# Kernel tuning notes

Hardware: AMD Instinct MI355X
Metric: run time of the kernel (lower is better)

## Reference

```python
import jax, jax.numpy as jnp
import numpy as np

N_NODES = 50000
N_EDGES = 800000
N_GRAPHS = 256
IN_DIM, HIDDEN_DIM, EMBED_DIM = 128, 64, 128


def setup_inputs() -> dict:
    key = jax.random.key(0)
    ks = jax.random.split(key, 8)
    x = jax.random.normal(ks[0], (N_NODES, IN_DIM), dtype=jnp.float32)
    edge_index = jax.random.randint(ks[1], (2, N_EDGES), 0, N_NODES, dtype=jnp.int64)
    edge_weight = jax.random.uniform(ks[2], (N_EDGES,), dtype=jnp.float32)
    batch_vec = jnp.sort(jax.random.randint(ks[3], (N_NODES,), 0, N_GRAPHS, dtype=jnp.int64))
    # Glorot-ish params for the two GCNConv layers
    W1 = jax.random.normal(ks[4], (IN_DIM, HIDDEN_DIM), dtype=jnp.float32) / np.sqrt(IN_DIM)
    b1 = jnp.zeros((HIDDEN_DIM,), dtype=jnp.float32)
    W2 = jax.random.normal(ks[5], (HIDDEN_DIM, EMBED_DIM), dtype=jnp.float32) / np.sqrt(HIDDEN_DIM)
    b2 = jnp.zeros((EMBED_DIM,), dtype=jnp.float32)
    return {"x": x, "edge_index": edge_index, "edge_weight": edge_weight,
            "batch_vec": batch_vec, "W1": W1, "b1": b1, "W2": W2, "b2": b2}


def _gcn_conv(x, src, dst, ew, W, b, num_nodes):
    # PyG GCNConv: linear transform, add self-loops (weight 1), sym-normalize, aggregate at dst.
    h = x @ W  # [N, out]
    loops = jnp.arange(num_nodes, dtype=src.dtype)
    row = jnp.concatenate([src, loops])
    col = jnp.concatenate([dst, loops])
    w = jnp.concatenate([ew, jnp.ones((num_nodes,), x.dtype)])
    deg = jax.ops.segment_sum(w, col, num_segments=num_nodes)
    dis = jnp.where(deg > 0, jax.lax.rsqrt(deg), 0.0)  # deg^{-1/2}, inf -> 0
    norm = dis[row] * w * dis[col]  # [E+N]
    msg = h[row] * norm[:, None]  # gather + scale
    out = jax.ops.segment_sum(msg, col, num_segments=num_nodes)  # scatter-add
    return out + b


def reference(x, edge_index, edge_weight, batch_vec, W1, b1, W2, b2):
    src, dst = edge_index[0], edge_index[1]
    h = jax.nn.relu(_gcn_conv(x, src, dst, edge_weight, W1, b1, N_NODES))
    # dropout is identity at inference
    h = jax.nn.relu(_gcn_conv(h, src, dst, edge_weight, W2, b2, N_NODES))
    # global_mean_pool over graphs
    s = jax.ops.segment_sum(h, batch_vec, num_segments=N_GRAPHS)
    cnt = jax.ops.segment_sum(jnp.ones((N_NODES,), h.dtype), batch_vec, num_segments=N_GRAPHS)
    return s / jnp.maximum(cnt, 1.0)[:, None]
```

## Files before the change

kernel.cpp:

```cpp
#include <hip/hip_runtime.h>

constexpr int N_NODES  = 50000;
constexpr int N_EDGES  = 800000;
constexpr int N_GRAPHS = 256;
constexpr int IN_DIM   = 128;
constexpr int HID      = 64;
constexpr int EMB      = 128;
constexpr int NBKT     = 196;
constexpr int EB       = (N_EDGES + 1023) / 1024;
constexpr int GB       = (N_NODES + 31) / 32;
constexpr int GSB      = (N_NODES + 255) / 256;
constexpr int NB2      = 64;

constexpr size_t OFF_POOL  = 0;
constexpr size_t OFF_GST   = 32768;
constexpr size_t OFF_BBASE = 33026;
constexpr size_t OFF_DIS   = 33224;
constexpr size_t OFF_RS    = 83224;
constexpr size_t OFF_HCNT  = 133224;
constexpr size_t OFF_REC   = 286496;
constexpr size_t OFF_PART  = OFF_REC + 2 * (size_t)N_EDGES;
constexpr size_t OFF_H1    = OFF_PART;
constexpr size_t OFF_H1P   = OFF_PART + 4 * (size_t)N_EDGES;
constexpr size_t OFF_AGG2  = OFF_H1P;

__device__ inline unsigned bf16r(float f) {
    unsigned u = __float_as_uint(f);
    return (u + 0x7fffu + ((u >> 16) & 1u)) >> 16;
}
__device__ inline unsigned bf16pack2(float lo, float hi) {
    return bf16r(lo) | (bf16r(hi) << 16);
}
__device__ inline float bflo(unsigned v) { return __uint_as_float(v << 16); }
__device__ inline float bfhi(unsigned v) { return __uint_as_float(v & 0xffff0000u); }

__device__ inline void fma4(float4& acc, float s, const float4& v) {
    acc.x += s * v.x; acc.y += s * v.y; acc.z += s * v.z; acc.w += s * v.w;
}

__global__ __launch_bounds__(256) void k_p1(const int* __restrict__ dst,
                                            int* __restrict__ hcnt) {
    __shared__ int lh[NBKT];
    int tid = threadIdx.x;
    for (int i = tid; i < NBKT; i += 256) lh[i] = 0;
    __syncthreads();
    int base = blockIdx.x * 1024;
    #pragma unroll
    for (int j = 0; j < 4; ++j) {
        int e = base + j * 256 + tid;
        if (e < N_EDGES) atomicAdd(&lh[dst[e] >> 8], 1);
    }
    __syncthreads();
    for (int i = tid; i < NBKT; i += 256) hcnt[blockIdx.x * NBKT + i] = lh[i];
}

__global__ __launch_bounds__(256) void k_kab(const int* __restrict__ hcnt,
                                             int* __restrict__ bbase) {
    __shared__ int tile[256];
    int t = threadIdx.x;
    int v = 0;
    if (t < NBKT) {
        for (int i = 0; i < EB; ++i) v += hcnt[i * NBKT + t];
    }
    tile[t] = v;
    __syncthreads();
    for (int off = 1; off < 256; off <<= 1) {
        int a = (t >= off) ? tile[t - off] : 0;
        __syncthreads();
        tile[t] += a;
        __syncthreads();
    }
    if (t < NBKT) bbase[t] = tile[t] - v;
    if (t == NBKT - 1) bbase[NBKT] = tile[t];
}

__global__ __launch_bounds__(256) void k_kc(int* __restrict__ hcnt,
                                            const int* __restrict__ bbase,
                                            const int* __restrict__ batch,
                                            int* __restrict__ gstart) {
    __shared__ int tile[256];
    __shared__ int carry;
    int t = threadIdx.x;
    if (blockIdx.x < NBKT) {
        int b = blockIdx.x;
        if (t == 0) carry = bbase[b];
        __syncthreads();
        for (int i0 = 0; i0 < EB; i0 += 256) {
            int i = i0 + t;
            int v = (i < EB) ? hcnt[i * NBKT + b] : 0;
            tile[t] = v;
            __syncthreads();
            for (int off = 1; off < 256; off <<= 1) {
                int a = (t >= off) ? tile[t - off] : 0;
                __syncthreads();
                tile[t] += a;
                __syncthreads();
            }
            int incl = tile[t];
            if (i < EB) hcnt[i * NBKT + b] = carry + incl - v;
            __syncthreads();
            if (t == 255) carry += incl;
            __syncthreads();
        }
        return;
    }
    int i = (blockIdx.x - NBKT) * 256 + t;
    if (i >= N_NODES) return;
    int g = batch[i];
    if (i == 0) {
        for (int gg = 0; gg <= g; ++gg) gstart[gg] = 0;
    } else {
        int gp = batch[i - 1];
        for (int gg = gp + 1; gg <= g; ++gg) gstart[gg] = i;
    }
    if (i == N_NODES - 1) {
        for (int gg = g + 1; gg <= N_GRAPHS; ++gg) gstart[gg] = N_NODES;
    }
}

__global__ __launch_bounds__(256) void k_p2(const int* __restrict__ src,
                                            const int* __restrict__ dst,
                                            const float* __restrict__ ew,
                                            const int* __restrict__ hcnt,
                                            uint4* __restrict__ part) {
    __shared__ int lb[NBKT];
    __shared__ int lc[NBKT];
    int tid = threadIdx.x;
    for (int i = tid; i < NBKT; i += 256) {
        lb[i] = hcnt[blockIdx.x * NBKT + i];
        lc[i] = 0;
    }
    __syncthreads();
    int base = blockIdx.x * 1024;
    #pragma unroll
    for (int j = 0; j < 4; ++j) {
        int e = base + j * 256 + tid;
        if (e < N_EDGES) {
            int d = dst[e];
            int b = d >> 8;
            int r = atomicAdd(&lc[b], 1);
            part[lb[b] + r] = make_uint4((unsigned)src[e], (unsigned)d,
                                         __float_as_uint(ew[e]), 0u);
        }
    }
}

__global__ __launch_bounds__(256) void k_p3_gemm1(const uint4* __restrict__ part,
                                                  const int* __restrict__ bbase,
                                                  int* __restrict__ rs,
                                                  float* __restrict__ dis,
                                                  uint2* __restrict__ rec,
                                                  const float* __restrict__ x,
                                                  const float* __restrict__ W1,
                                                  unsigned* __restrict__ h) {
    __shared__ float Ws[IN_DIM * HID];
    __shared__ float xs[32][IN_DIM + 4];
    __shared__ int   cnt[256];
    __shared__ float dgw[256];
    __shared__ int   scn[256];
    __shared__ int   cur[256];
    int tid = threadIdx.x;
    if (blockIdx.x < NBKT) {
        int b = blockIdx.x;
        int base_node = b << 8;
        int ebeg = bbase[b], eend = bbase[b + 1];
        cnt[tid] = 0;
        dgw[tid] = 0.f;
        __syncthreads();
        for (int e = ebeg + tid; e < eend; e += 256) {
            uint4 r = part[e];
            int ld = (int)r.y & 255;
            atomicAdd(&cnt[ld], 1);
            atomicAdd(&dgw[ld], __uint_as_float(r.z));
        }
        __syncthreads();
        scn[tid] = cnt[tid];
        __syncthreads();
        for (int off = 1; off < 256; off <<= 1) {
            int a = (tid >= off) ? scn[tid - off] : 0;
            __syncthreads();
            scn[tid] += a;
            __syncthreads();
        }
        int node = base_node + tid;
        if (node < N_NODES) {
            rs[node] = ebeg + scn[tid];
            dis[node] = rsqrtf(dgw[tid] + 1.0f);
        }
        cur[tid] = ebeg + scn[tid] - cnt[tid];
        __syncthreads();
        for (int e = ebeg + tid; e < eend; e += 256) {
            uint4 r = part[e];
            int ld = (int)r.y & 255;
            int pos = atomicAdd(&cur[ld], 1);
            rec[pos] = make_uint2(r.x, r.z);
        }
        return;
    }
    int bid = blockIdx.x - NBKT;
    const float4* W4 = (const float4*)W1;
    float4* Ws4 = (float4*)Ws;
    for (int i = tid; i < IN_DIM * HID / 4; i += 256) Ws4[i] = W4[i];
    int base = bid * 32;
    const float4* X4 = (const float4*)x;
    for (int i = tid; i < 32 * 32; i += 256) {
        int ln = i >> 5, kq = i & 31;
        int node = base + ln;
        float4 v = (node < N_NODES) ? X4[(size_t)node * 32 + kq]
                                    : make_float4(0.f, 0.f, 0.f, 0.f);
        *(float4*)&xs[ln][kq * 4] = v;
    }
    __syncthreads();
    int np = tid >> 4;
    int q  = tid & 15;
    int n0 = np * 2, n1 = n0 + 1;
    float4 a0 = make_float4(0.f, 0.f, 0.f, 0.f);
    float4 a1 = a0;
    #pragma unroll 4
    for (int k4 = 0; k4 < IN_DIM; k4 += 4) {
        float4 xv0 = *(const float4*)&xs[n0][k4];
        float4 xv1 = *(const float4*)&xs[n1][k4];
        float4 w0 = Ws4[(k4 + 0) * 16 + q];
        float4 w1 = Ws4[(k4 + 1) * 16 + q];
        float4 w2 = Ws4[(k4 + 2) * 16 + q];
        float4 w3 = Ws4[(k4 + 3) * 16 + q];
        fma4(a0, xv0.x, w0); fma4(a0, xv0.y, w1); fma4(a0, xv0.z, w2); fma4(a0, xv0.w, w3);
        fma4(a1, xv1.x, w0); fma4(a1, xv1.y, w1); fma4(a1, xv1.z, w2); fma4(a1, xv1.w, w3);
    }
    int nd0 = base + n0, nd1 = base + n1;
    if (nd0 < N_NODES) {
        uint2 p = make_uint2(bf16pack2(a0.x, a0.y), bf16pack2(a0.z, a0.w));
        ((uint2*)h)[(size_t)nd0 * 16 + q] = p;
    }
    if (nd1 < N_NODES) {
        uint2 p = make_uint2(bf16pack2(a1.x, a1.y), bf16pack2(a1.z, a1.w));
        ((uint2*)h)[(size_t)nd1 * 16 + q] = p;
    }
}

template <bool RELU_BIAS, bool OUT_BF16>
__global__ __launch_bounds__(256) void k_gather64(const uint2* __restrict__ rec,
                                                  const int* __restrict__ rs,
                                                  const float* __restrict__ dis,
                                                  const unsigned* __restrict__ T,
                                                  const float* __restrict__ bias,
                                                  void* __restrict__ outv) {
    int wave = (blockIdx.x * 256 + threadIdx.x) >> 6;
    int lane = threadIdx.x & 63;
    int half = lane >> 5;
    int l    = lane & 31;
    if (wave >= N_NODES) return;
    int n = wave;
    int begin = (n == 0) ? 0 : rs[n - 1];
    int end = rs[n];

    float ax0 = 0.f, ay0 = 0.f, ax1 = 0.f, ay1 = 0.f;
    float ax2 = 0.f, ay2 = 0.f, ax3 = 0.f, ay3 = 0.f;
    int k = begin + half;
    while (k + 6 < end) {
        uint2 r0 = rec[k];
        uint2 r1 = rec[k + 2];
        uint2 r2 = rec[k + 4];
        uint2 r3 = rec[k + 6];
        float d0 = dis[r0.x];
        float d1 = dis[r1.x];
        float d2 = dis[r2.x];
        float d3 = dis[r3.x];
        unsigned t0 = T[(size_t)r0.x * 32 + l];
        unsigned t1 = T[(size_t)r1.x * 32 + l];
        unsigned t2 = T[(size_t)r2.x * 32 + l];
        unsigned t3 = T[(size_t)r3.x * 32 + l];
        float n0 = d0 * __uint_as_float(r0.y);
        float n1 = d1 * __uint_as_float(r1.y);
        float n2 = d2 * __uint_as_float(r2.y);
        float n3 = d3 * __uint_as_float(r3.y);
        ax0 += bflo(t0) * n0; ay0 += bfhi(t0) * n0;
        ax1 += bflo(t1) * n1; ay1 += bfhi(t1) * n1;
        ax2 += bflo(t2) * n2; ay2 += bfhi(t2) * n2;
        ax3 += bflo(t3) * n3; ay3 += bfhi(t3) * n3;
        k += 8;
    }
    while (k < end) {
        uint2 r = rec[k];
        float nn = dis[r.x] * __uint_as_float(r.y);
        unsigned t = T[(size_t)r.x * 32 + l];
        ax0 += bflo(t) * nn; ay0 += bfhi(t) * nn;
        k += 2;
    }
    float ax = (ax0 + ax1) + (ax2 + ax3);
    float ay = (ay0 + ay1) + (ay2 + ay3);
    float di = dis[n];
    if (half == 0) {
        unsigned t = T[(size_t)n * 32 + l];
        ax += bflo(t) * di; ay += bfhi(t) * di;
    }
    ax += __shfl_xor(ax, 32, 64);
    ay += __shfl_xor(ay, 32, 64);
    if (half == 0) {
        ax *= di; ay *= di;
        if (RELU_BIAS) {
            const float2* B2 = (const float2*)bias;
            float2 b = B2[l];
            ax += b.x; ay += b.y;
            ax = ax > 0.f ? ax : 0.f;
            ay = ay > 0.f ? ay : 0.f;
        }
        if (OUT_BF16) {
            ((unsigned*)outv)[(size_t)n * 32 + l] = bf16pack2(ax, ay);
        } else {
            ((float2*)outv)[(size_t)n * 32 + l] = make_float2(ax, ay);
        }
    }
}

__global__ __launch_bounds__(256) void k_gemm2_pool(const float* __restrict__ agg,
                                                    const float* __restrict__ W2,
                                                    const float* __restrict__ b2,
                                                    const int* __restrict__ batch,
                                                    float* __restrict__ pool) {
    __shared__ float Ws[HID * EMB];
    __shared__ float as[NB2][HID];
    __shared__ int   bs[NB2];
    int tid = threadIdx.x;
    const float4* W4 = (const float4*)W2;
    float4* Ws4 = (float4*)Ws;
    for (int i = tid; i < HID * EMB / 4; i += 256) Ws4[i] = W4[i];
    int base = blockIdx.x * NB2;
    const float4* A4 = (const float4*)agg;
    float4* as4 = (float4*)as;
    for (int i = tid; i < NB2 * HID / 4; i += 256) {
        int node = base + (i >> 4);
        as4[i] = (node < N_NODES) ? A4[(size_t)node * 16 + (i & 15)]
                                  : make_float4(0.f, 0.f, 0.f, 0.f);
    }
    if (tid < NB2) {
        int node = base + tid;
        bs[tid] = (node < N_NODES) ? batch[node] : -1;
    }
    __syncthreads();

    int c = tid & 31;
    int s = tid >> 5;
    int jc = c * 4;
    int nb = s * 8;
    float4 acc[8];
    #pragma unroll
    for (int i = 0; i < 8; ++i) acc[i] = make_float4(0.f, 0.f, 0.f, 0.f);
    #pragma unroll 4
    for (int k4 = 0; k4 < HID; k4 += 4) {
        float4 w0 = Ws4[(k4 + 0) * 32 + c];
        float4 w1 = Ws4[(k4 + 1) * 32 + c];
        float4 w2 = Ws4[(k4 + 2) * 32 + c];
        float4 w3 = Ws4[(k4 + 3) * 32 + c];
        #pragma unroll
        for (int i = 0; i < 8; ++i) {
            float4 av = *(const float4*)&as[nb + i][k4];
            fma4(acc[i], av.x, w0); fma4(acc[i], av.y, w1);
            fma4(acc[i], av.z, w2); fma4(acc[i], av.w, w3);
        }
    }
    float4 bq = *(const float4*)&b2[jc];
    float4 racc = make_float4(0.f, 0.f, 0.f, 0.f);
    int gcur = -1;
    #pragma unroll
    for (int i = 0; i < 8; ++i) {
        int g = bs[nb + i];
        if (g != gcur) {
            if (gcur >= 0) {
                float* p = &pool[(size_t)gcur * EMB + jc];
                atomicAdd(p + 0, racc.x); atomicAdd(p + 1, racc.y);
                atomicAdd(p + 2, racc.z); atomicAdd(p + 3, racc.w);
            }
            racc = make_float4(0.f, 0.f, 0.f, 0.f);
            gcur = g;
        }
        if (g < 0) continue;
        racc.x += fmaxf(acc[i].x + bq.x, 0.f);
        racc.y += fmaxf(acc[i].y + bq.y, 0.f);
        racc.z += fmaxf(acc[i].z + bq.z, 0.f);
        racc.w += fmaxf(acc[i].w + bq.w, 0.f);
    }
    if (gcur >= 0) {
        float* p = &pool[(size_t)gcur * EMB + jc];
        atomicAdd(p + 0, racc.x); atomicAdd(p + 1, racc.y);
        atomicAdd(p + 2, racc.z); atomicAdd(p + 3, racc.w);
    }
}

__global__ void k_divide(const float* __restrict__ pool, const int* __restrict__ gstart,
                         float* __restrict__ out) {
    int idx = blockIdx.x * blockDim.x + threadIdx.x;
    if (idx >= N_GRAPHS * EMB) return;
    int g = idx >> 7;
    float c = (float)(gstart[g + 1] - gstart[g]);
    out[idx] = pool[idx] / fmaxf(c, 1.0f);
}

extern "C" void kernel_launch(void* const* d_in, const int* in_sizes, int n_in,
                              void* d_out, int out_size, void* d_ws, size_t ws_size,
                              hipStream_t stream) {
    const float* x     = (const float*)d_in[0];
    const int*   eidx  = (const int*)d_in[1];
    const float* ew    = (const float*)d_in[2];
    const int*   batch = (const int*)d_in[3];
    const float* W1    = (const float*)d_in[4];
    const float* b1    = (const float*)d_in[5];
    const float* W2    = (const float*)d_in[6];
    const float* b2    = (const float*)d_in[7];
    float* out = (float*)d_out;

    const int* src = eidx;
    const int* dst = eidx + N_EDGES;

    float* ws     = (float*)d_ws;
    float* pool   = ws + OFF_POOL;
    int*   gstart = (int*)(ws + OFF_GST);
    int*   bbase  = (int*)(ws + OFF_BBASE);
    float* dis    = ws + OFF_DIS;
    int*   rs     = (int*)(ws + OFF_RS);
    int*   hcnt   = (int*)(ws + OFF_HCNT);
    uint2* rec    = (uint2*)(ws + OFF_REC);
    uint4* part   = (uint4*)(ws + OFF_PART);
    unsigned* h1  = (unsigned*)(ws + OFF_H1);
    unsigned* h1p = (unsigned*)(ws + OFF_H1P);
    float* agg2   = ws + OFF_AGG2;

    (void)hipMemsetAsync(pool, 0, (size_t)N_GRAPHS * EMB * sizeof(float), stream);

    k_p1<<<EB, 256, 0, stream>>>(dst, hcnt);
    k_kab<<<1, 256, 0, stream>>>(hcnt, bbase);
    k_kc<<<NBKT + GSB, 256, 0, stream>>>(hcnt, bbase, batch, gstart);
    k_p2<<<EB, 256, 0, stream>>>(src, dst, ew, hcnt, part);

    k_p3_gemm1<<<NBKT + GB, 256, 0, stream>>>(part, bbase, rs, dis, rec, x, W1, h1p);

    k_gather64<true, true><<<N_NODES / 4, 256, 0, stream>>>(rec, rs, dis, h1p, b1, h1);

    k_gather64<false, false><<<N_NODES / 4, 256, 0, stream>>>(rec, rs, dis, h1, nullptr, agg2);

    k_gemm2_pool<<<(N_NODES + NB2 - 1) / NB2, 256, 0, stream>>>(agg2, W2, b2, batch, pool);

    k_divide<<<(N_GRAPHS * EMB + 255) / 256, 256, 0, stream>>>(pool, gstart, out);
}
```

Baseline: 252.1 us.

## Split SpMM gathers into two column-half passes with four edge lanes per wave

Each 64-column gather kernel becomes two launches, and each launch handles a 32-column half of the bf16 feature table. Within a wave, 16 lanes cover the columns and four groups of lanes stride across edges. The aim is to shrink the gathered table's working set per pass so it fits better in cache, and to give more edge-level parallelism per node. In exchange, the edge records and dis values are read twice, each gathered row is a smaller 64-byte fragment, and two extra kernel launches are added.

```diff
diff --git a/kernel.cpp b/kernel.cpp
--- a/kernel.cpp
+++ b/kernel.cpp
@@ -238,8 +238,8 @@
     }
 }
 
-template <bool RELU_BIAS, bool OUT_BF16>
-__global__ __launch_bounds__(256) void k_gather64(const uint2* __restrict__ rec,
+template <bool RELU_BIAS, bool OUT_BF16, int COLH>
+__global__ __launch_bounds__(256) void k_gather32(const uint2* __restrict__ rec,
                                                   const int* __restrict__ rs,
                                                   const float* __restrict__ dis,
                                                   const unsigned* __restrict__ T,
@@ -247,68 +247,59 @@
                                                   void* __restrict__ outv) {
     int wave = (blockIdx.x * 256 + threadIdx.x) >> 6;
     int lane = threadIdx.x & 63;
-    int half = lane >> 5;
-    int l    = lane & 31;
+    int q    = lane >> 4;
+    int l    = lane & 15;
     if (wave >= N_NODES) return;
     int n = wave;
     int begin = (n == 0) ? 0 : rs[n - 1];
     int end = rs[n];
+    const unsigned* Th = T + COLH * 16;
 
     float ax0 = 0.f, ay0 = 0.f, ax1 = 0.f, ay1 = 0.f;
-    float ax2 = 0.f, ay2 = 0.f, ax3 = 0.f, ay3 = 0.f;
-    int k = begin + half;
-    while (k + 6 < end) {
+    int k = begin + q;
+    while (k + 4 < end) {
         uint2 r0 = rec[k];
-        uint2 r1 = rec[k + 2];
-        uint2 r2 = rec[k + 4];
-        uint2 r3 = rec[k + 6];
+        uint2 r1 = rec[k + 4];
         float d0 = dis[r0.x];
         float d1 = dis[r1.x];
-        float d2 = dis[r2.x];
-        float d3 = dis[r3.x];
-        unsigned t0 = T[(size_t)r0.x * 32 + l];
-        unsigned t1 = T[(size_t)r1.x * 32 + l];
-        unsigned t2 = T[(size_t)r2.x * 32 + l];
-        unsigned t3 = T[(size_t)r3.x * 32 + l];
+        unsigned t0 = Th[(size_t)r0.x * 32 + l];
+        unsigned t1 = Th[(size_t)r1.x * 32 + l];
         float n0 = d0 * __uint_as_float(r0.y);
         float n1 = d1 * __uint_as_float(r1.y);
-        float n2 = d2 * __uint_as_float(r2.y);
-        float n3 = d3 * __uint_as_float(r3.y);
         ax0 += bflo(t0) * n0; ay0 += bfhi(t0) * n0;
         ax1 += bflo(t1) * n1; ay1 += bfhi(t1) * n1;
-        ax2 += bflo(t2) * n2; ay2 += bfhi(t2) * n2;
-        ax3 += bflo(t3) * n3; ay3 += bfhi(t3) * n3;
         k += 8;
     }
     while (k < end) {
         uint2 r = rec[k];
         float nn = dis[r.x] * __uint_as_float(r.y);
-        unsigned t = T[(size_t)r.x * 32 + l];
+        unsigned t = Th[(size_t)r.x * 32 + l];
         ax0 += bflo(t) * nn; ay0 += bfhi(t) * nn;
-        k += 2;
-    }
-    float ax = (ax0 + ax1) + (ax2 + ax3);
-    float ay = (ay0 + ay1) + (ay2 + ay3);
+        k += 4;
+    }
+    float ax = ax0 + ax1, ay = ay0 + ay1;
     float di = dis[n];
-    if (half == 0) {
-        unsigned t = T[(size_t)n * 32 + l];
+    if (q == 0) {
+        unsigned t = Th[(size_t)n * 32 + l];
         ax += bflo(t) * di; ay += bfhi(t) * di;
     }
+    ax += __shfl_xor(ax, 16, 64);
+    ay += __shfl_xor(ay, 16, 64);
     ax += __shfl_xor(ax, 32, 64);
     ay += __shfl_xor(ay, 32, 64);
-    if (half == 0) {
+    if (q == 0) {
         ax *= di; ay *= di;
         if (RELU_BIAS) {
             const float2* B2 = (const float2*)bias;
-            float2 b = B2[l];
+            float2 b = B2[COLH * 16 + l];
             ax += b.x; ay += b.y;
             ax = ax > 0.f ? ax : 0.f;
             ay = ay > 0.f ? ay : 0.f;
         }
         if (OUT_BF16) {
-            ((unsigned*)outv)[(size_t)n * 32 + l] = bf16pack2(ax, ay);
+            ((unsigned*)outv)[(size_t)n * 32 + COLH * 16 + l] = bf16pack2(ax, ay);
         } else {
-            ((float2*)outv)[(size_t)n * 32 + l] = make_float2(ax, ay);
+            ((float2*)outv)[(size_t)n * 32 + COLH * 16 + l] = make_float2(ax, ay);
         }
     }
 }
@@ -434,9 +425,11 @@
 
     k_p3_gemm1<<<NBKT + GB, 256, 0, stream>>>(part, bbase, rs, dis, rec, x, W1, h1p);
 
-    k_gather64<true, true><<<N_NODES / 4, 256, 0, stream>>>(rec, rs, dis, h1p, b1, h1);
-
-    k_gather64<false, false><<<N_NODES / 4, 256, 0, stream>>>(rec, rs, dis, h1, nullptr, agg2);
+    k_gather32<true, true, 0><<<N_NODES / 4, 256, 0, stream>>>(rec, rs, dis, h1p, b1, h1);
+    k_gather32<true, true, 1><<<N_NODES / 4, 256, 0, stream>>>(rec, rs, dis, h1p, b1, h1);
+
+    k_gather32<false, false, 0><<<N_NODES / 4, 256, 0, stream>>>(rec, rs, dis, h1, nullptr, agg2);
+    k_gather32<false, false, 1><<<N_NODES / 4, 256, 0, stream>>>(rec, rs, dis, h1, nullptr, agg2);
 
     k_gemm2_pool<<<(N_NODES + NB2 - 1) / NB2, 256, 0, stream>>>(agg2, W2, b2, batch, pool);
 
```

Result: slower. 291.1 us (+15.5%).
